# Optimization experiments

Measured on AMD Instinct MI355X. Metric: run time of the kernel, lower is better.

The kernel has to match this reference:

```python
import jax, jax.numpy as jnp
import numpy as np

B_, L, S_IN, S_OUT, Z_IN, Z_OUT = 2, 768, 1280, 32, 1, 32
D_INNER, D_STATE, D_CONV, DT_RANK = 64, 16, 4, 2  # expand=2 -> d_inner=64; dt_rank=ceil(32/16)=2


def setup_inputs() -> dict:
    key = jax.random.key(0)
    ks = jax.random.split(key, 12)
    p = lambda i, shape, scale=0.02: jax.random.normal(ks[i], shape, jnp.float32) * scale
    return dict(
        s=jax.random.normal(ks[0], (B_, L, S_IN), jnp.float32),
        z=jax.random.normal(ks[1], (B_, L, L, Z_IN), jnp.float32),
        s_proj_w=p(2, (S_OUT, S_IN)), s_proj_b=jnp.zeros((S_OUT,), jnp.float32),
        z_proj_w=p(3, (Z_OUT, Z_IN)), z_proj_b=jnp.zeros((Z_OUT,), jnp.float32),
        in_proj_w=p(4, (2 * D_INNER, S_OUT)),
        conv_w=p(5, (D_INNER, D_CONV)), conv_b=jnp.zeros((D_INNER,), jnp.float32),
        x_proj_w=p(6, (DT_RANK + 2 * D_STATE, D_INNER)),
        dt_proj_w=p(7, (D_INNER, DT_RANK)), dt_proj_b=p(8, (D_INNER,), 1.0),
        A_log=jnp.log(jnp.broadcast_to(jnp.arange(1, D_STATE + 1, dtype=jnp.float32), (D_INNER, D_STATE))),
        D=jnp.ones((D_INNER,), jnp.float32),
        out_proj_w=p(9, (S_OUT, D_INNER)),
    )


def mamba(u, in_proj_w, conv_w, conv_b, x_proj_w, dt_proj_w, dt_proj_b, A_log, D, out_proj_w):
    # u: [b, l, d_model]
    b, l, _ = u.shape
    xz = u @ in_proj_w.T                      # [b, l, 2*d_inner]
    x, gate = jnp.split(xz, 2, axis=-1)
    # causal depthwise conv1d, kernel D_CONV, then SiLU
    xp = jnp.pad(x, ((0, 0), (D_CONV - 1, 0), (0, 0)))
    x = sum(xp[:, k:k + l, :] * conv_w[:, k] for k in range(D_CONV)) + conv_b
    x = jax.nn.silu(x)
    x_dbl = x @ x_proj_w.T                    # [b, l, dt_rank + 2*d_state]
    dt, Bm, Cm = jnp.split(x_dbl, [DT_RANK, DT_RANK + D_STATE], axis=-1)
    dt = jax.nn.softplus(dt @ dt_proj_w.T + dt_proj_b)   # [b, l, d_inner]
    A = -jnp.exp(A_log)                       # [d_inner, d_state]
    dA = jnp.exp(dt[..., None] * A)           # [b, l, d, n]
    dBu = dt[..., None] * Bm[:, :, None, :] * x[..., None]  # [b, l, d, n]

    def step(h, ins):
        dA_t, dBu_t, C_t = ins
        h = dA_t * h + dBu_t                  # [b, d, n]
        return h, jnp.einsum('bdn,bn->bd', h, C_t)

    h0 = jnp.zeros((b, D_INNER, D_STATE), u.dtype)
    _, ys = jax.lax.scan(step, h0, (jnp.swapaxes(dA, 0, 1), jnp.swapaxes(dBu, 0, 1), jnp.swapaxes(Cm, 0, 1)))
    y = jnp.swapaxes(ys, 0, 1) + x * D        # D skip connection
    y = y * jax.nn.silu(gate)                 # gated output
    return y @ out_proj_w.T                   # [b, l, d_model]


def reference(s, z, s_proj_w, s_proj_b, z_proj_w, z_proj_b, in_proj_w, conv_w, conv_b,
              x_proj_w, dt_proj_w, dt_proj_b, A_log, D, out_proj_w):
    s_prime = s @ s_proj_w.T + s_proj_b                       # [b, l, 32]
    s_prime = mamba(s_prime, in_proj_w, conv_w, conv_b, x_proj_w,
                    dt_proj_w, dt_proj_b, A_log, D, out_proj_w)
    z_prime = z @ z_proj_w.T + z_proj_b                       # [b, l, l, 32]
    z_prime = z_prime + jnp.einsum('bsf,btf->bstf', s_prime, s_prime)
    return (s_prime, z_prime)
```

## Files before the change

kernel.cpp:

```cpp
#include <hip/hip_runtime.h>
#include <math.h>

#define B_     2
#define L_     768
#define SIN_   1280
#define SOUT_  32
#define DI_    64
#define DST_   16
#define DCONV_ 4
#define DTR_   2
#define NCH    48
#define CH     16


__global__ __launch_bounds__(256) void k_sproj(
    const float* __restrict__ s, const float* __restrict__ spw,
    const float* __restrict__ spb, const float* __restrict__ ipw,
    float* __restrict__ xz)
{
    __shared__ float srow[4][SIN_];
    __shared__ float w2[2 * DI_ * SOUT_];
    __shared__ float u[4][SOUT_];
    const int tid = threadIdx.x;
    const int row0 = blockIdx.x * 4;

    for (int r = 0; r < 4; ++r) {
        const float* src = s + (long)(row0 + r) * SIN_;
        for (int i = tid; i < SIN_; i += 256) srow[r][i] = src[i];
    }
    for (int i = tid; i < 2 * DI_ * SOUT_; i += 256) w2[i] = ipw[i];
    __syncthreads();

    const int f = tid >> 3;
    const int c = tid & 7;
    float p0 = 0.f, p1 = 0.f, p2 = 0.f, p3 = 0.f;
    const float* wrow = spw + (long)f * SIN_;
    for (int k = c; k < SIN_; k += 8) {
        float w = wrow[k];
        p0 += srow[0][k] * w; p1 += srow[1][k] * w;
        p2 += srow[2][k] * w; p3 += srow[3][k] * w;
    }
    #pragma unroll
    for (int m = 1; m <= 4; m <<= 1) {
        p0 += __shfl_xor(p0, m); p1 += __shfl_xor(p1, m);
        p2 += __shfl_xor(p2, m); p3 += __shfl_xor(p3, m);
    }
    if (c == 0) {
        float b = spb[f];
        u[0][f] = p0 + b; u[1][f] = p1 + b;
        u[2][f] = p2 + b; u[3][f] = p3 + b;
    }
    __syncthreads();

    const int j  = tid & 127;
    const int rh = tid >> 7;
    #pragma unroll
    for (int rp = 0; rp < 2; ++rp) {
        int r = rp * 2 + rh;
        float acc = 0.f;
        const float* wj = &w2[j * SOUT_];
        #pragma unroll
        for (int k = 0; k < SOUT_; ++k) acc += u[r][k] * wj[k];
        xz[(long)(row0 + r) * 128 + j] = acc;
    }
}

__global__ __launch_bounds__(256) void k_pre(
    const float* __restrict__ xz, const float* __restrict__ convw,
    const float* __restrict__ convb, const float* __restrict__ xpw,
    const float* __restrict__ dtw, const float* __restrict__ dtb,
    float* __restrict__ xs_out, float* __restrict__ dtf,
    float* __restrict__ dtx, float* __restrict__ Bws, float* __restrict__ Cws)
{
    const int row0 = blockIdx.x * 4;
    const int tid = threadIdx.x;
    const int r = tid >> 6, d = tid & 63;
    const int row = row0 + r;
    const int b = row / L_, l = row - b * L_;
    __shared__ float sxpw[64][34];
    __shared__ float sdtw[128];
    __shared__ float sxs[4][DI_];
    __shared__ float sxd[4][34];

    for (int i = tid; i < 34 * 64; i += 256) {
        int j = i >> 6, k = i & 63;
        sxpw[k][j] = xpw[i];
    }
    if (tid < 128) sdtw[tid] = dtw[tid];

    float xc = convb[d];
    #pragma unroll
    for (int k = 0; k < DCONV_; ++k) {
        int ls = l + k - (DCONV_ - 1);
        if (ls >= 0) xc = fmaf(xz[(long)(b * L_ + ls) * 128 + d], convw[d * 4 + k], xc);
    }
    float xsv = xc / (1.f + expf(-xc));
    sxs[r][d] = xsv;
    xs_out[(long)row * DI_ + d] = xsv;
    __syncthreads();

    if (d < DTR_ + 2 * DST_) {
        float acc = 0.f;
        #pragma unroll
        for (int k = 0; k < 64; ++k) acc = fmaf(sxs[r][k], sxpw[k][d], acc);
        sxd[r][d] = acc;
    }
    __syncthreads();

    if (d < DST_) {
        Bws[(long)row * DST_ + d] = sxd[r][DTR_ + d];
        Cws[(long)row * DST_ + d] = sxd[r][DTR_ + DST_ + d];
    }
    float dtv = fmaf(sxd[r][0], sdtw[d * 2], fmaf(sxd[r][1], sdtw[d * 2 + 1], dtb[d]));
    dtv = dtv > 20.f ? dtv : log1pf(expf(dtv));
    dtf[(long)row * DI_ + d] = dtv;
    dtx[(long)row * DI_ + d] = dtv * xsv;
}

__global__ __launch_bounds__(64) void k_scan_p1(
    const float* __restrict__ dtf, const float* __restrict__ dtx,
    const float* __restrict__ Bws, const float* __restrict__ Alog,
    float* __restrict__ Pst, float* __restrict__ Lst)
{
    const int bc = blockIdx.x;
    const int b = bc / NCH, c = bc - b * NCH;
    const int d = threadIdx.x;
    __shared__ float sB[CH * 16];
    const long base = (long)b * L_ + c * CH;
    ((float4*)sB)[d] = ((const float4*)(Bws + base * DST_))[d];

    float A2[DST_], P[DST_], hl[DST_];
    #pragma unroll
    for (int n = 0; n < DST_; ++n) {
        A2[n] = -expf(Alog[d * DST_ + n]) * 1.44269504088896f;
        P[n] = 1.f; hl[n] = 0.f;
    }
    __syncthreads();

    #pragma unroll
    for (int l = 0; l < CH; ++l) {
        float dt = dtf[(base + l) * DI_ + d];
        float dx = dtx[(base + l) * DI_ + d];
        #pragma unroll
        for (int n = 0; n < DST_; ++n) {
            float a = exp2f(dt * A2[n]);
            P[n] *= a;
            hl[n] = fmaf(a, hl[n], dx * sB[l * 16 + n]);
        }
    }
    float4* Pp = (float4*)(Pst + ((long)bc * 64 + d) * 16);
    float4* Lp = (float4*)(Lst + ((long)bc * 64 + d) * 16);
    #pragma unroll
    for (int q = 0; q < 4; ++q) {
        Pp[q] = ((float4*)P)[q];
        Lp[q] = ((float4*)hl)[q];
    }
}

__global__ __launch_bounds__(256) void k_scan_p2(
    const float* __restrict__ Pst, const float* __restrict__ Lst,
    float* __restrict__ Hst)
{
    const int idx = blockIdx.x * 256 + threadIdx.x;
    const int b = idx >> 10, e = idx & 1023;
    float H = 0.f;
    #pragma unroll 8
    for (int c = 0; c < NCH; ++c) {
        long o = ((long)(b * NCH + c)) * 1024 + e;
        Hst[o] = H;
        H = fmaf(Pst[o], H, Lst[o]);
    }
}

__global__ __launch_bounds__(64) void k_scan_p3(
    const float* __restrict__ dtf, const float* __restrict__ dtx,
    const float* __restrict__ Bws, const float* __restrict__ Cws,
    const float* __restrict__ Alog, const float* __restrict__ Hst,
    float* __restrict__ ysc)
{
    const int bc = blockIdx.x;
    const int b = bc / NCH, c = bc - b * NCH;
    const int d = threadIdx.x;
    __shared__ float sB[CH * 16], sC[CH * 16];
    const long base = (long)b * L_ + c * CH;
    ((float4*)sB)[d] = ((const float4*)(Bws + base * DST_))[d];
    ((float4*)sC)[d] = ((const float4*)(Cws + base * DST_))[d];

    float A2[DST_], h[DST_];
    #pragma unroll
    for (int n = 0; n < DST_; ++n)
        A2[n] = -expf(Alog[d * DST_ + n]) * 1.44269504088896f;
    const float4* Hp = (const float4*)(Hst + ((long)bc * 64 + d) * 16);
    #pragma unroll
    for (int q = 0; q < 4; ++q) ((float4*)h)[q] = Hp[q];
    __syncthreads();

    #pragma unroll
    for (int l = 0; l < CH; ++l) {
        float dt = dtf[(base + l) * DI_ + d];
        float dx = dtx[(base + l) * DI_ + d];
        float y = 0.f;
        #pragma unroll
        for (int n = 0; n < DST_; ++n) {
            float a = exp2f(dt * A2[n]);
            h[n] = fmaf(a, h[n], dx * sB[l * 16 + n]);
            y = fmaf(h[n], sC[l * 16 + n], y);
        }
        ysc[(base + l) * DI_ + d] = y;
    }
}

__global__ __launch_bounds__(256) void k_epi(
    const float* __restrict__ ysc, const float* __restrict__ xs,
    const float* __restrict__ xz, const float* __restrict__ Dv,
    const float* __restrict__ opw, float* __restrict__ sp)
{
    const int row0 = blockIdx.x * 4;
    const int tid = threadIdx.x;
    const int r = tid >> 6, d = tid & 63;
    const int row = row0 + r;
    __shared__ float sy[4][DI_];
    __shared__ float sw[64][SOUT_];

    for (int i = tid; i < SOUT_ * DI_; i += 256) {
        int f = i >> 6, k = i & 63;
        sw[k][f] = opw[i];
    }
    float g = xz[(long)row * 128 + DI_ + d];
    float yv = fmaf(xs[(long)row * DI_ + d], Dv[d], ysc[(long)row * DI_ + d]);
    yv *= g / (1.f + expf(-g));
    sy[r][d] = yv;
    __syncthreads();

    if (d < SOUT_) {
        float acc = 0.f;
        #pragma unroll
        for (int k = 0; k < DI_; ++k) acc = fmaf(sy[r][k], sw[k][d], acc);
        sp[(long)row * SOUT_ + d] = acc;
    }
}

__global__ __launch_bounds__(256) void k_z(
    const float* __restrict__ z, const float* __restrict__ zw,
    const float* __restrict__ zb, const float* __restrict__ sp,
    float* __restrict__ zout)
{
    const int idx = blockIdx.x * 256 + threadIdx.x;
    const int bs  = idx / 6144;
    const int rem = idx - bs * 6144;
    const int t   = rem >> 3;
    const int f4  = rem & 7;
    const int b   = bs / L_;

    float zval = z[(long)bs * L_ + t];
    float4 w4 = ((const float4*)zw)[f4];
    float4 b4 = ((const float4*)zb)[f4];
    float4 ss = ((const float4*)sp)[bs * 8 + f4];
    float4 st = ((const float4*)sp)[(b * L_ + t) * 8 + f4];
    float4 o;
    o.x = zval * w4.x + b4.x + ss.x * st.x;
    o.y = zval * w4.y + b4.y + ss.y * st.y;
    o.z = zval * w4.z + b4.z + ss.z * st.z;
    o.w = zval * w4.w + b4.w + ss.w * st.w;
    ((float4*)zout)[(long)idx] = o;
}

extern "C" void kernel_launch(void* const* d_in, const int* in_sizes, int n_in,
                              void* d_out, int out_size, void* d_ws, size_t ws_size,
                              hipStream_t stream) {
    const float* s     = (const float*)d_in[0];
    const float* z     = (const float*)d_in[1];
    const float* spw   = (const float*)d_in[2];
    const float* spb   = (const float*)d_in[3];
    const float* zw    = (const float*)d_in[4];
    const float* zb    = (const float*)d_in[5];
    const float* ipw   = (const float*)d_in[6];
    const float* convw = (const float*)d_in[7];
    const float* convb = (const float*)d_in[8];
    const float* xpw   = (const float*)d_in[9];
    const float* dtw   = (const float*)d_in[10];
    const float* dtb   = (const float*)d_in[11];
    const float* Alog  = (const float*)d_in[12];
    const float* Dv    = (const float*)d_in[13];
    const float* opw   = (const float*)d_in[14];

    float* out = (float*)d_out;
    float* ws  = (float*)d_ws;
    float* xz  = ws;
    float* xs  = ws + 196608;
    float* dtf = ws + 294912;
    float* dtx = ws + 393216;
    float* Bws = ws + 491520;
    float* Cws = ws + 516096;
    float* ysc = ws + 540672;
    float* Pst = ws + 638976;
    float* Lst = ws + 737280;
    float* Hst = ws + 835584;

    float* sp   = out;
    float* zout = out + 49152;

    k_sproj  <<<(B_ * L_) / 4, 256, 0, stream>>>(s, spw, spb, ipw, xz);
    k_pre    <<<(B_ * L_) / 4, 256, 0, stream>>>(xz, convw, convb, xpw, dtw, dtb,
                                                 xs, dtf, dtx, Bws, Cws);
    k_scan_p1<<<B_ * NCH, 64, 0, stream>>>(dtf, dtx, Bws, Alog, Pst, Lst);
    k_scan_p2<<<8, 256, 0, stream>>>(Pst, Lst, Hst);
    k_scan_p3<<<B_ * NCH, 64, 0, stream>>>(dtf, dtx, Bws, Cws, Alog, Hst, ysc);
    k_epi    <<<(B_ * L_) / 4, 256, 0, stream>>>(ysc, xs, xz, Dv, opw, sp);
    k_z      <<<(B_ * L_ * L_ * 8) / 256, 256, 0, stream>>>(z, zw, zb, sp, zout);
}
```

Measured before the change: 284.7 us.

## Fuse projection, conv, and scan phases into chunk-based front/back kernels

Merges the s-projection, in-projection, conv/SiLU, x-projection/dt, and chunk-local scan pass into one per-chunk kernel. It also merges the scan output pass with the gated D-skip and out-projection into a second per-chunk kernel, cutting seven launches to four and removing the xz and ysc intermediates. The cost is a smaller grid of 96 blocks, so the 1280-wide s-projection now runs on far fewer CUs, and it recomputes 3 halo rows per chunk. The z broadcast kernel, which likely dominates total time, is unchanged.

```diff
diff --git a/kernel.cpp b/kernel.cpp
--- a/kernel.cpp
+++ b/kernel.cpp
@@ -13,151 +13,168 @@
 #define CH     16
 
 
-__global__ __launch_bounds__(256) void k_sproj(
+__global__ __launch_bounds__(256) void k_front(
     const float* __restrict__ s, const float* __restrict__ spw,
     const float* __restrict__ spb, const float* __restrict__ ipw,
-    float* __restrict__ xz)
+    const float* __restrict__ convw, const float* __restrict__ convb,
+    const float* __restrict__ xpw, const float* __restrict__ dtw,
+    const float* __restrict__ dtb, const float* __restrict__ Alog,
+    float* __restrict__ gate_o, float* __restrict__ xs_o,
+    float* __restrict__ dtf_o, float* __restrict__ dtx_o,
+    float* __restrict__ Bws, float* __restrict__ Cws,
+    float* __restrict__ Pst, float* __restrict__ Lst)
 {
-    __shared__ float srow[4][SIN_];
-    __shared__ float w2[2 * DI_ * SOUT_];
-    __shared__ float u[4][SOUT_];
+    const int bc  = blockIdx.x;
+    const int b   = bc / NCH, c = bc - b * NCH;
+    const int l0  = c * CH;
     const int tid = threadIdx.x;
-    const int row0 = blockIdx.x * 4;
-
-    for (int r = 0; r < 4; ++r) {
-        const float* src = s + (long)(row0 + r) * SIN_;
-        for (int i = tid; i < SIN_; i += 256) srow[r][i] = src[i];
-    }
-    for (int i = tid; i < 2 * DI_ * SOUT_; i += 256) w2[i] = ipw[i];
-    __syncthreads();
-
-    const int f = tid >> 3;
-    const int c = tid & 7;
-    float p0 = 0.f, p1 = 0.f, p2 = 0.f, p3 = 0.f;
-    const float* wrow = spw + (long)f * SIN_;
-    for (int k = c; k < SIN_; k += 8) {
-        float w = wrow[k];
-        p0 += srow[0][k] * w; p1 += srow[1][k] * w;
-        p2 += srow[2][k] * w; p3 += srow[3][k] * w;
-    }
-    #pragma unroll
-    for (int m = 1; m <= 4; m <<= 1) {
-        p0 += __shfl_xor(p0, m); p1 += __shfl_xor(p1, m);
-        p2 += __shfl_xor(p2, m); p3 += __shfl_xor(p3, m);
-    }
-    if (c == 0) {
-        float b = spb[f];
-        u[0][f] = p0 + b; u[1][f] = p1 + b;
-        u[2][f] = p2 + b; u[3][f] = p3 + b;
-    }
-    __syncthreads();
-
-    const int j  = tid & 127;
-    const int rh = tid >> 7;
-    #pragma unroll
-    for (int rp = 0; rp < 2; ++rp) {
-        int r = rp * 2 + rh;
-        float acc = 0.f;
-        const float* wj = &w2[j * SOUT_];
-        #pragma unroll
-        for (int k = 0; k < SOUT_; ++k) acc += u[r][k] * wj[k];
-        xz[(long)(row0 + r) * 128 + j] = acc;
-    }
-}
-
-__global__ __launch_bounds__(256) void k_pre(
-    const float* __restrict__ xz, const float* __restrict__ convw,
-    const float* __restrict__ convb, const float* __restrict__ xpw,
-    const float* __restrict__ dtw, const float* __restrict__ dtb,
-    float* __restrict__ xs_out, float* __restrict__ dtf,
-    float* __restrict__ dtx, float* __restrict__ Bws, float* __restrict__ Cws)
-{
-    const int row0 = blockIdx.x * 4;
-    const int tid = threadIdx.x;
-    const int r = tid >> 6, d = tid & 63;
-    const int row = row0 + r;
-    const int b = row / L_, l = row - b * L_;
+
+    __shared__ float sw2[128 * 33];
     __shared__ float sxpw[64][34];
     __shared__ float sdtw[128];
-    __shared__ float sxs[4][DI_];
-    __shared__ float sxd[4][34];
-
-    for (int i = tid; i < 34 * 64; i += 256) {
-        int j = i >> 6, k = i & 63;
-        sxpw[k][j] = xpw[i];
-    }
+    __shared__ float srow[4][SIN_];
+    __shared__ float su[20][SOUT_];
+    __shared__ float sx[20][DI_];
+    __shared__ float sxs[CH][DI_];
+    __shared__ float sxd[CH][34];
+    __shared__ float sdtf[CH][DI_];
+    __shared__ float sdtx[CH][DI_];
+    __shared__ float sB[CH][DST_];
+
+    for (int i = tid; i < 128 * 32; i += 256)
+        sw2[(i >> 5) * 33 + (i & 31)] = ipw[i];
+    for (int i = tid; i < 34 * 64; i += 256)
+        sxpw[i & 63][i >> 6] = xpw[i];
     if (tid < 128) sdtw[tid] = dtw[tid];
 
-    float xc = convb[d];
-    #pragma unroll
-    for (int k = 0; k < DCONV_; ++k) {
-        int ls = l + k - (DCONV_ - 1);
-        if (ls >= 0) xc = fmaf(xz[(long)(b * L_ + ls) * 128 + d], convw[d * 4 + k], xc);
-    }
-    float xsv = xc / (1.f + expf(-xc));
-    sxs[r][d] = xsv;
-    xs_out[(long)row * DI_ + d] = xsv;
-    __syncthreads();
-
-    if (d < DTR_ + 2 * DST_) {
+    const int f  = tid >> 3;
+    const int cc = tid & 7;
+    for (int g = 0; g < 5; ++g) {
+        for (int rr = 0; rr < 4; ++rr) {
+            int l = l0 - 3 + g * 4 + rr;
+            if (l >= 0 && l < L_) {
+                const float* src = s + ((long)(b * L_ + l)) * SIN_;
+                for (int i = tid; i < SIN_; i += 256) srow[rr][i] = src[i];
+            } else {
+                for (int i = tid; i < SIN_; i += 256) srow[rr][i] = 0.f;
+            }
+        }
+        __syncthreads();
+        float p0 = 0.f, p1 = 0.f, p2 = 0.f, p3 = 0.f;
+        const float* wrow = spw + (long)f * SIN_;
+        for (int k = cc; k < SIN_; k += 8) {
+            float w = wrow[k];
+            p0 += srow[0][k] * w; p1 += srow[1][k] * w;
+            p2 += srow[2][k] * w; p3 += srow[3][k] * w;
+        }
+        #pragma unroll
+        for (int m = 1; m <= 4; m <<= 1) {
+            p0 += __shfl_xor(p0, m); p1 += __shfl_xor(p1, m);
+            p2 += __shfl_xor(p2, m); p3 += __shfl_xor(p3, m);
+        }
+        if (cc == 0) {
+            float bb = spb[f];
+            #pragma unroll
+            for (int rr = 0; rr < 4; ++rr) {
+                int l = l0 - 3 + g * 4 + rr;
+                float pv = (rr == 0) ? p0 : (rr == 1) ? p1 : (rr == 2) ? p2 : p3;
+                su[g * 4 + rr][f] = (l >= 0 && l < L_) ? pv + bb : 0.f;
+            }
+        }
+        __syncthreads();
+    }
+
+    for (int i = tid; i < 19 * 64; i += 256) {
+        int si = i >> 6, j = i & 63;
+        const float* w = &sw2[j * 33];
         float acc = 0.f;
         #pragma unroll
-        for (int k = 0; k < 64; ++k) acc = fmaf(sxs[r][k], sxpw[k][d], acc);
-        sxd[r][d] = acc;
-    }
-    __syncthreads();
-
-    if (d < DST_) {
-        Bws[(long)row * DST_ + d] = sxd[r][DTR_ + d];
-        Cws[(long)row * DST_ + d] = sxd[r][DTR_ + DST_ + d];
-    }
-    float dtv = fmaf(sxd[r][0], sdtw[d * 2], fmaf(sxd[r][1], sdtw[d * 2 + 1], dtb[d]));
-    dtv = dtv > 20.f ? dtv : log1pf(expf(dtv));
-    dtf[(long)row * DI_ + d] = dtv;
-    dtx[(long)row * DI_ + d] = dtv * xsv;
-}
-
-__global__ __launch_bounds__(64) void k_scan_p1(
-    const float* __restrict__ dtf, const float* __restrict__ dtx,
-    const float* __restrict__ Bws, const float* __restrict__ Alog,
-    float* __restrict__ Pst, float* __restrict__ Lst)
-{
-    const int bc = blockIdx.x;
-    const int b = bc / NCH, c = bc - b * NCH;
-    const int d = threadIdx.x;
-    __shared__ float sB[CH * 16];
-    const long base = (long)b * L_ + c * CH;
-    ((float4*)sB)[d] = ((const float4*)(Bws + base * DST_))[d];
-
-    float A2[DST_], P[DST_], hl[DST_];
-    #pragma unroll
-    for (int n = 0; n < DST_; ++n) {
-        A2[n] = -expf(Alog[d * DST_ + n]) * 1.44269504088896f;
-        P[n] = 1.f; hl[n] = 0.f;
-    }
-    __syncthreads();
-
-    #pragma unroll
-    for (int l = 0; l < CH; ++l) {
-        float dt = dtf[(base + l) * DI_ + d];
-        float dx = dtx[(base + l) * DI_ + d];
+        for (int k = 0; k < SOUT_; ++k) acc += su[si][k] * w[k];
+        sx[si][j] = acc;
+    }
+    for (int i = tid; i < CH * 64; i += 256) {
+        int r = i >> 6, j = i & 63;
+        const float* w = &sw2[(64 + j) * 33];
+        float acc = 0.f;
+        #pragma unroll
+        for (int k = 0; k < SOUT_; ++k) acc += su[r + 3][k] * w[k];
+        gate_o[((long)(b * L_ + l0 + r)) * DI_ + j] = acc;
+    }
+    __syncthreads();
+
+    for (int i = tid; i < CH * DI_; i += 256) {
+        int r = i >> 6, d = i & 63;
+        float xc = convb[d];
+        #pragma unroll
+        for (int k = 0; k < DCONV_; ++k)
+            xc = fmaf(sx[r + k][d], convw[d * 4 + k], xc);
+        float xv = xc / (1.f + expf(-xc));
+        sxs[r][d] = xv;
+        xs_o[((long)(b * L_ + l0 + r)) * DI_ + d] = xv;
+    }
+    __syncthreads();
+
+    for (int i = tid; i < CH * 34; i += 256) {
+        int r = i / 34, o = i - r * 34;
+        float acc = 0.f;
+        #pragma unroll
+        for (int k = 0; k < DI_; ++k) acc = fmaf(sxs[r][k], sxpw[k][o], acc);
+        sxd[r][o] = acc;
+    }
+    __syncthreads();
+
+    for (int i = tid; i < CH * DI_; i += 256) {
+        int r = i >> 6, d = i & 63;
+        float dtv = fmaf(sxd[r][0], sdtw[2 * d], fmaf(sxd[r][1], sdtw[2 * d + 1], dtb[d]));
+        dtv = dtv > 20.f ? dtv : log1pf(expf(dtv));
+        float xv = sxs[r][d];
+        sdtf[r][d] = dtv;
+        sdtx[r][d] = dtv * xv;
+        long o = ((long)(b * L_ + l0 + r)) * DI_ + d;
+        dtf_o[o] = dtv;
+        dtx_o[o] = dtv * xv;
+    }
+    {
+        int r = tid >> 4, n = tid & 15;
+        float Bv = sxd[r][DTR_ + n];
+        float Cv = sxd[r][DTR_ + DST_ + n];
+        sB[r][n] = Bv;
+        long o = ((long)(b * L_ + l0 + r)) * DST_ + n;
+        Bws[o] = Bv;
+        Cws[o] = Cv;
+    }
+    __syncthreads();
+
+    if (tid < 64) {
+        const int d = tid;
+        float A2[DST_], P[DST_], hl[DST_];
         #pragma unroll
         for (int n = 0; n < DST_; ++n) {
-            float a = exp2f(dt * A2[n]);
-            P[n] *= a;
-            hl[n] = fmaf(a, hl[n], dx * sB[l * 16 + n]);
-        }
-    }
-    float4* Pp = (float4*)(Pst + ((long)bc * 64 + d) * 16);
-    float4* Lp = (float4*)(Lst + ((long)bc * 64 + d) * 16);
-    #pragma unroll
-    for (int q = 0; q < 4; ++q) {
-        Pp[q] = ((float4*)P)[q];
-        Lp[q] = ((float4*)hl)[q];
-    }
-}
-
-__global__ __launch_bounds__(256) void k_scan_p2(
+            A2[n] = -expf(Alog[d * DST_ + n]) * 1.44269504088896f;
+            P[n] = 1.f; hl[n] = 0.f;
+        }
+        #pragma unroll
+        for (int l = 0; l < CH; ++l) {
+            float dt = sdtf[l][d];
+            float dx = sdtx[l][d];
+            #pragma unroll
+            for (int n = 0; n < DST_; ++n) {
+                float a = exp2f(dt * A2[n]);
+                P[n] *= a;
+                hl[n] = fmaf(a, hl[n], dx * sB[l][n]);
+            }
+        }
+        float4* Pp = (float4*)(Pst + ((long)bc * 64 + d) * 16);
+        float4* Lp = (float4*)(Lst + ((long)bc * 64 + d) * 16);
+        #pragma unroll
+        for (int q = 0; q < 4; ++q) {
+            Pp[q] = ((float4*)P)[q];
+            Lp[q] = ((float4*)hl)[q];
+        }
+    }
+}
+
+__global__ __launch_bounds__(256) void k_carry(
     const float* __restrict__ Pst, const float* __restrict__ Lst,
     float* __restrict__ Hst)
 {
@@ -172,71 +189,76 @@
     }
 }
 
-__global__ __launch_bounds__(64) void k_scan_p3(
+__global__ __launch_bounds__(256) void k_back(
     const float* __restrict__ dtf, const float* __restrict__ dtx,
     const float* __restrict__ Bws, const float* __restrict__ Cws,
     const float* __restrict__ Alog, const float* __restrict__ Hst,
-    float* __restrict__ ysc)
+    const float* __restrict__ xs, const float* __restrict__ gate,
+    const float* __restrict__ Dv, const float* __restrict__ opw,
+    float* __restrict__ sp)
 {
-    const int bc = blockIdx.x;
-    const int b = bc / NCH, c = bc - b * NCH;
-    const int d = threadIdx.x;
-    __shared__ float sB[CH * 16], sC[CH * 16];
-    const long base = (long)b * L_ + c * CH;
-    ((float4*)sB)[d] = ((const float4*)(Bws + base * DST_))[d];
-    ((float4*)sC)[d] = ((const float4*)(Cws + base * DST_))[d];
-
-    float A2[DST_], h[DST_];
-    #pragma unroll
-    for (int n = 0; n < DST_; ++n)
-        A2[n] = -expf(Alog[d * DST_ + n]) * 1.44269504088896f;
-    const float4* Hp = (const float4*)(Hst + ((long)bc * 64 + d) * 16);
-    #pragma unroll
-    for (int q = 0; q < 4; ++q) ((float4*)h)[q] = Hp[q];
-    __syncthreads();
-
-    #pragma unroll
-    for (int l = 0; l < CH; ++l) {
-        float dt = dtf[(base + l) * DI_ + d];
-        float dx = dtx[(base + l) * DI_ + d];
-        float y = 0.f;
-        #pragma unroll
-        for (int n = 0; n < DST_; ++n) {
-            float a = exp2f(dt * A2[n]);
-            h[n] = fmaf(a, h[n], dx * sB[l * 16 + n]);
-            y = fmaf(h[n], sC[l * 16 + n], y);
-        }
-        ysc[(base + l) * DI_ + d] = y;
-    }
-}
-
-__global__ __launch_bounds__(256) void k_epi(
-    const float* __restrict__ ysc, const float* __restrict__ xs,
-    const float* __restrict__ xz, const float* __restrict__ Dv,
-    const float* __restrict__ opw, float* __restrict__ sp)
-{
-    const int row0 = blockIdx.x * 4;
+    const int bc  = blockIdx.x;
+    const int b   = bc / NCH, c = bc - b * NCH;
+    const int l0  = c * CH;
     const int tid = threadIdx.x;
-    const int r = tid >> 6, d = tid & 63;
-    const int row = row0 + r;
-    __shared__ float sy[4][DI_];
-    __shared__ float sw[64][SOUT_];
-
-    for (int i = tid; i < SOUT_ * DI_; i += 256) {
-        int f = i >> 6, k = i & 63;
-        sw[k][f] = opw[i];
-    }
-    float g = xz[(long)row * 128 + DI_ + d];
-    float yv = fmaf(xs[(long)row * DI_ + d], Dv[d], ysc[(long)row * DI_ + d]);
-    yv *= g / (1.f + expf(-g));
-    sy[r][d] = yv;
-    __syncthreads();
-
-    if (d < SOUT_) {
+    const long rbase = (long)(b * L_ + l0);
+
+    __shared__ float sB[CH][DST_], sC[CH][DST_];
+    __shared__ float sdtf[CH][DI_], sdtx[CH][DI_];
+    __shared__ float sy[CH][DI_];
+    __shared__ float sw[DI_][SOUT_];
+
+    for (int i = tid; i < CH * DST_; i += 256) {
+        sB[i >> 4][i & 15] = Bws[rbase * DST_ + i];
+        sC[i >> 4][i & 15] = Cws[rbase * DST_ + i];
+    }
+    for (int i = tid; i < CH * DI_; i += 256) {
+        sdtf[i >> 6][i & 63] = dtf[rbase * DI_ + i];
+        sdtx[i >> 6][i & 63] = dtx[rbase * DI_ + i];
+    }
+    for (int i = tid; i < SOUT_ * DI_; i += 256)
+        sw[i & 63][i >> 6] = opw[i];
+    __syncthreads();
+
+    if (tid < 64) {
+        const int d = tid;
+        float A2[DST_], h[DST_];
+        #pragma unroll
+        for (int n = 0; n < DST_; ++n)
+            A2[n] = -expf(Alog[d * DST_ + n]) * 1.44269504088896f;
+        const float4* Hp = (const float4*)(Hst + ((long)bc * 64 + d) * 16);
+        #pragma unroll
+        for (int q = 0; q < 4; ++q) ((float4*)h)[q] = Hp[q];
+        #pragma unroll
+        for (int l = 0; l < CH; ++l) {
+            float dt = sdtf[l][d];
+            float dx = sdtx[l][d];
+            float y = 0.f;
+            #pragma unroll
+            for (int n = 0; n < DST_; ++n) {
+                float a = exp2f(dt * A2[n]);
+                h[n] = fmaf(a, h[n], dx * sB[l][n]);
+                y = fmaf(h[n], sC[l][n], y);
+            }
+            sy[l][d] = y;
+        }
+    }
+    __syncthreads();
+
+    for (int i = tid; i < CH * DI_; i += 256) {
+        int r = i >> 6, d = i & 63;
+        float g  = gate[(rbase + r) * DI_ + d];
+        float yv = fmaf(xs[(rbase + r) * DI_ + d], Dv[d], sy[r][d]);
+        sy[r][d] = yv * (g / (1.f + expf(-g)));
+    }
+    __syncthreads();
+
+    for (int i = tid; i < CH * SOUT_; i += 256) {
+        int r = i >> 5, o = i & 31;
         float acc = 0.f;
         #pragma unroll
-        for (int k = 0; k < DI_; ++k) acc = fmaf(sy[r][k], sw[k][d], acc);
-        sp[(long)row * SOUT_ + d] = acc;
+        for (int k = 0; k < DI_; ++k) acc = fmaf(sy[r][k], sw[k][o], acc);
+        sp[(rbase + r) * SOUT_ + o] = acc;
     }
 }
 
@@ -284,28 +306,26 @@
     const float* Dv    = (const float*)d_in[13];
     const float* opw   = (const float*)d_in[14];
 
-    float* out = (float*)d_out;
-    float* ws  = (float*)d_ws;
-    float* xz  = ws;
-    float* xs  = ws + 196608;
-    float* dtf = ws + 294912;
-    float* dtx = ws + 393216;
-    float* Bws = ws + 491520;
-    float* Cws = ws + 516096;
-    float* ysc = ws + 540672;
-    float* Pst = ws + 638976;
-    float* Lst = ws + 737280;
-    float* Hst = ws + 835584;
+    float* out  = (float*)d_out;
+    float* ws   = (float*)d_ws;
+    float* gate = ws;
+    float* xs   = ws + 98304;
+    float* dtf  = ws + 196608;
+    float* dtx  = ws + 294912;
+    float* Bws  = ws + 393216;
+    float* Cws  = ws + 417792;
+    float* Pst  = ws + 442368;
+    float* Lst  = ws + 540672;
+    float* Hst  = ws + 638976;
 
     float* sp   = out;
     float* zout = out + 49152;
 
-    k_sproj  <<<(B_ * L_) / 4, 256, 0, stream>>>(s, spw, spb, ipw, xz);
-    k_pre    <<<(B_ * L_) / 4, 256, 0, stream>>>(xz, convw, convb, xpw, dtw, dtb,
-                                                 xs, dtf, dtx, Bws, Cws);
-    k_scan_p1<<<B_ * NCH, 64, 0, stream>>>(dtf, dtx, Bws, Alog, Pst, Lst);
-    k_scan_p2<<<8, 256, 0, stream>>>(Pst, Lst, Hst);
-    k_scan_p3<<<B_ * NCH, 64, 0, stream>>>(dtf, dtx, Bws, Cws, Alog, Hst, ysc);
-    k_epi    <<<(B_ * L_) / 4, 256, 0, stream>>>(ysc, xs, xz, Dv, opw, sp);
-    k_z      <<<(B_ * L_ * L_ * 8) / 256, 256, 0, stream>>>(z, zw, zb, sp, zout);
-}
+    k_front<<<B_ * NCH, 256, 0, stream>>>(s, spw, spb, ipw, convw, convb, xpw,
+                                          dtw, dtb, Alog, gate, xs, dtf, dtx,
+                                          Bws, Cws, Pst, Lst);
+    k_carry<<<8, 256, 0, stream>>>(Pst, Lst, Hst);
+    k_back <<<B_ * NCH, 256, 0, stream>>>(dtf, dtx, Bws, Cws, Alog, Hst,
+                                          xs, gate, Dv, opw, sp);
+    k_z    <<<(B_ * L_ * L_ * 8) / 256, 256, 0, stream>>>(z, zw, zb, sp, zout);
+}
```

New measurement: 351.9 us. 23.6% more time.

## Parallelize scan over state dim and fuse scan pass 3 with epilogue

Applied to the files above, without the earlier changes.

The chunked scan kernels now assign one thread per (channel, state) pair instead of looping over 16 states per thread, which raises thread count and cuts register pressure. The third scan pass is fused with the gating/out-projection epilogue, with a shuffle reduction over the state dim, removing the ysc round-trip and one launch. k_sproj also gets float4 loads and padded shared weights to avoid bank conflicts. The cost is a 1024-thread block with more shared memory, and shuffle reductions added to the inner loop.

```diff
diff --git a/kernel.cpp b/kernel.cpp
--- a/kernel.cpp
+++ b/kernel.cpp
@@ -19,16 +19,18 @@
     float* __restrict__ xz)
 {
     __shared__ float srow[4][SIN_];
-    __shared__ float w2[2 * DI_ * SOUT_];
+    __shared__ float w2[128 * 33];
     __shared__ float u[4][SOUT_];
     const int tid = threadIdx.x;
     const int row0 = blockIdx.x * 4;
 
     for (int r = 0; r < 4; ++r) {
-        const float* src = s + (long)(row0 + r) * SIN_;
-        for (int i = tid; i < SIN_; i += 256) srow[r][i] = src[i];
-    }
-    for (int i = tid; i < 2 * DI_ * SOUT_; i += 256) w2[i] = ipw[i];
+        const float4* src = (const float4*)(s + (long)(row0 + r) * SIN_);
+        for (int i = tid; i < SIN_ / 4; i += 256)
+            ((float4*)srow[r])[i] = src[i];
+    }
+    for (int i = tid; i < 128 * 32; i += 256)
+        w2[(i >> 5) * 33 + (i & 31)] = ipw[i];
     __syncthreads();
 
     const int f = tid >> 3;
@@ -58,7 +60,7 @@
     for (int rp = 0; rp < 2; ++rp) {
         int r = rp * 2 + rh;
         float acc = 0.f;
-        const float* wj = &w2[j * SOUT_];
+        const float* wj = &w2[j * 33];
         #pragma unroll
         for (int k = 0; k < SOUT_; ++k) acc += u[r][k] * wj[k];
         xz[(long)(row0 + r) * 128 + j] = acc;
@@ -117,44 +119,43 @@
     dtx[(long)row * DI_ + d] = dtv * xsv;
 }
 
-__global__ __launch_bounds__(64) void k_scan_p1(
+__global__ __launch_bounds__(256) void k_scan_p1(
     const float* __restrict__ dtf, const float* __restrict__ dtx,
     const float* __restrict__ Bws, const float* __restrict__ Alog,
     float* __restrict__ Pst, float* __restrict__ Lst)
 {
-    const int bc = blockIdx.x;
-    const int b = bc / NCH, c = bc - b * NCH;
-    const int d = threadIdx.x;
-    __shared__ float sB[CH * 16];
+    const int blk = blockIdx.x;
+    const int dq  = blk & 3;
+    const int bc  = blk >> 2;
+    const int b   = bc / NCH, c = bc - b * NCH;
+    const int tid = threadIdx.x;
+    const int dl  = tid >> 4, n = tid & 15;
+    const int d   = dq * 16 + dl;
     const long base = (long)b * L_ + c * CH;
-    ((float4*)sB)[d] = ((const float4*)(Bws + base * DST_))[d];
-
-    float A2[DST_], P[DST_], hl[DST_];
-    #pragma unroll
-    for (int n = 0; n < DST_; ++n) {
-        A2[n] = -expf(Alog[d * DST_ + n]) * 1.44269504088896f;
-        P[n] = 1.f; hl[n] = 0.f;
-    }
+
+    __shared__ float sB[CH][16];
+    __shared__ float sdt[CH][16];
+    __shared__ float sdx[CH][16];
+
+    if (tid < 64) ((float4*)sB)[tid] = ((const float4*)(Bws + base * DST_))[tid];
+    {
+        int l = tid >> 4, j = tid & 15;
+        sdt[l][j] = dtf[(base + l) * DI_ + dq * 16 + j];
+        sdx[l][j] = dtx[(base + l) * DI_ + dq * 16 + j];
+    }
+    float A2 = -expf(Alog[d * DST_ + n]) * 1.44269504088896f;
+    float P = 1.f, hl = 0.f;
     __syncthreads();
 
     #pragma unroll
     for (int l = 0; l < CH; ++l) {
-        float dt = dtf[(base + l) * DI_ + d];
-        float dx = dtx[(base + l) * DI_ + d];
-        #pragma unroll
-        for (int n = 0; n < DST_; ++n) {
-            float a = exp2f(dt * A2[n]);
-            P[n] *= a;
-            hl[n] = fmaf(a, hl[n], dx * sB[l * 16 + n]);
-        }
-    }
-    float4* Pp = (float4*)(Pst + ((long)bc * 64 + d) * 16);
-    float4* Lp = (float4*)(Lst + ((long)bc * 64 + d) * 16);
-    #pragma unroll
-    for (int q = 0; q < 4; ++q) {
-        Pp[q] = ((float4*)P)[q];
-        Lp[q] = ((float4*)hl)[q];
-    }
+        float a = exp2f(sdt[l][dl] * A2);
+        P *= a;
+        hl = fmaf(a, hl, sdx[l][dl] * sB[l][n]);
+    }
+    long o = (long)bc * 1024 + dq * 256 + tid;
+    Pst[o] = P;
+    Lst[o] = hl;
 }
 
 __global__ __launch_bounds__(256) void k_scan_p2(
@@ -172,71 +173,67 @@
     }
 }
 
-__global__ __launch_bounds__(64) void k_scan_p3(
+__global__ __launch_bounds__(1024) void k_back(
     const float* __restrict__ dtf, const float* __restrict__ dtx,
     const float* __restrict__ Bws, const float* __restrict__ Cws,
     const float* __restrict__ Alog, const float* __restrict__ Hst,
-    float* __restrict__ ysc)
-{
-    const int bc = blockIdx.x;
-    const int b = bc / NCH, c = bc - b * NCH;
-    const int d = threadIdx.x;
-    __shared__ float sB[CH * 16], sC[CH * 16];
+    const float* __restrict__ xs, const float* __restrict__ xz,
+    const float* __restrict__ Dv, const float* __restrict__ opw,
+    float* __restrict__ sp)
+{
+    const int bc  = blockIdx.x;
+    const int b   = bc / NCH, c = bc - b * NCH;
+    const int tid = threadIdx.x;
     const long base = (long)b * L_ + c * CH;
-    ((float4*)sB)[d] = ((const float4*)(Bws + base * DST_))[d];
-    ((float4*)sC)[d] = ((const float4*)(Cws + base * DST_))[d];
-
-    float A2[DST_], h[DST_];
-    #pragma unroll
-    for (int n = 0; n < DST_; ++n)
-        A2[n] = -expf(Alog[d * DST_ + n]) * 1.44269504088896f;
-    const float4* Hp = (const float4*)(Hst + ((long)bc * 64 + d) * 16);
-    #pragma unroll
-    for (int q = 0; q < 4; ++q) ((float4*)h)[q] = Hp[q];
+
+    __shared__ float sB[CH][16], sC[CH][16];
+    __shared__ float sdt[CH][64], sdx[CH][64];
+    __shared__ float sy[CH][65];
+    __shared__ float sw[64][33];
+
+    if (tid < 64) {
+        ((float4*)sB)[tid] = ((const float4*)(Bws + base * DST_))[tid];
+        ((float4*)sC)[tid] = ((const float4*)(Cws + base * DST_))[tid];
+    }
+    {
+        int l = tid >> 6, dd = tid & 63;
+        sdt[l][dd] = dtf[(base + l) * DI_ + dd];
+        sdx[l][dd] = dtx[(base + l) * DI_ + dd];
+    }
+    if (tid < SOUT_ * DI_) sw[tid & 63][tid >> 6] = opw[tid];
+
+    const int d = tid >> 4, n = tid & 15;
+    float A2 = -expf(Alog[d * DST_ + n]) * 1.44269504088896f;
+    float h = Hst[(long)bc * 1024 + tid];
     __syncthreads();
 
     #pragma unroll
     for (int l = 0; l < CH; ++l) {
-        float dt = dtf[(base + l) * DI_ + d];
-        float dx = dtx[(base + l) * DI_ + d];
-        float y = 0.f;
-        #pragma unroll
-        for (int n = 0; n < DST_; ++n) {
-            float a = exp2f(dt * A2[n]);
-            h[n] = fmaf(a, h[n], dx * sB[l * 16 + n]);
-            y = fmaf(h[n], sC[l * 16 + n], y);
-        }
-        ysc[(base + l) * DI_ + d] = y;
-    }
-}
-
-__global__ __launch_bounds__(256) void k_epi(
-    const float* __restrict__ ysc, const float* __restrict__ xs,
-    const float* __restrict__ xz, const float* __restrict__ Dv,
-    const float* __restrict__ opw, float* __restrict__ sp)
-{
-    const int row0 = blockIdx.x * 4;
-    const int tid = threadIdx.x;
-    const int r = tid >> 6, d = tid & 63;
-    const int row = row0 + r;
-    __shared__ float sy[4][DI_];
-    __shared__ float sw[64][SOUT_];
-
-    for (int i = tid; i < SOUT_ * DI_; i += 256) {
-        int f = i >> 6, k = i & 63;
-        sw[k][f] = opw[i];
-    }
-    float g = xz[(long)row * 128 + DI_ + d];
-    float yv = fmaf(xs[(long)row * DI_ + d], Dv[d], ysc[(long)row * DI_ + d]);
-    yv *= g / (1.f + expf(-g));
-    sy[r][d] = yv;
-    __syncthreads();
-
-    if (d < SOUT_) {
+        float a = exp2f(sdt[l][d] * A2);
+        h = fmaf(a, h, sdx[l][d] * sB[l][n]);
+        float y = h * sC[l][n];
+        y += __shfl_xor(y, 1);
+        y += __shfl_xor(y, 2);
+        y += __shfl_xor(y, 4);
+        y += __shfl_xor(y, 8);
+        if (n == 0) sy[l][d] = y;
+    }
+    __syncthreads();
+
+    {
+        int r = tid >> 6, dd = tid & 63;
+        float g  = xz[(base + r) * 128 + DI_ + dd];
+        float yv = fmaf(xs[(base + r) * DI_ + dd], Dv[dd], sy[r][dd]);
+        sy[r][dd] = yv * (g / (1.f + expf(-g)));
+    }
+    __syncthreads();
+
+    if (tid < CH * SOUT_) {
+        int r = tid >> 5, o = tid & 31;
         float acc = 0.f;
         #pragma unroll
-        for (int k = 0; k < DI_; ++k) acc = fmaf(sy[r][k], sw[k][d], acc);
-        sp[(long)row * SOUT_ + d] = acc;
+        for (int k = 0; k < DI_; ++k) acc = fmaf(sy[r][k], sw[k][o], acc);
+        sp[(base + r) * SOUT_ + o] = acc;
     }
 }
 
@@ -292,10 +289,9 @@
     float* dtx = ws + 393216;
     float* Bws = ws + 491520;
     float* Cws = ws + 516096;
-    float* ysc = ws + 540672;
-    float* Pst = ws + 638976;
-    float* Lst = ws + 737280;
-    float* Hst = ws + 835584;
+    float* Pst = ws + 540672;
+    float* Lst = ws + 638976;
+    float* Hst = ws + 737280;
 
     float* sp   = out;
     float* zout = out + 49152;
@@ -303,9 +299,9 @@
     k_sproj  <<<(B_ * L_) / 4, 256, 0, stream>>>(s, spw, spb, ipw, xz);
     k_pre    <<<(B_ * L_) / 4, 256, 0, stream>>>(xz, convw, convb, xpw, dtw, dtb,
                                                  xs, dtf, dtx, Bws, Cws);
-    k_scan_p1<<<B_ * NCH, 64, 0, stream>>>(dtf, dtx, Bws, Alog, Pst, Lst);
+    k_scan_p1<<<B_ * NCH * 4, 256, 0, stream>>>(dtf, dtx, Bws, Alog, Pst, Lst);
     k_scan_p2<<<8, 256, 0, stream>>>(Pst, Lst, Hst);
-    k_scan_p3<<<B_ * NCH, 64, 0, stream>>>(dtf, dtx, Bws, Cws, Alog, Hst, ysc);
-    k_epi    <<<(B_ * L_) / 4, 256, 0, stream>>>(ysc, xs, xz, Dv, opw, sp);
+    k_back   <<<B_ * NCH, 1024, 0, stream>>>(dtf, dtx, Bws, Cws, Alog, Hst,
+                                             xs, xz, Dv, opw, sp);
     k_z      <<<(B_ * L_ * L_ * 8) / 256, 256, 0, stream>>>(z, zw, zb, sp, zout);
 }
```

New measurement: 260.8 us. 1.09x faster.
